# Performance work log

Measured on AMD Instinct MI355X. Metric: run time of the kernel, lower is better.

Reference implementation:

```python
import jax, jax.numpy as jnp
import numpy as np

E = 768      # embed_size
H = 12       # heads
L = 4        # num_length (stacked blocks)
N = 3072     # sequence length (and max_length)
FF = 4 * E   # feed-forward hidden
EPS = 1e-5


def layer_norm(x, g, b):
    mu = jnp.mean(x, axis=-1, keepdims=True)
    var = jnp.mean((x - mu) ** 2, axis=-1, keepdims=True)
    return (x - mu) / jnp.sqrt(var + EPS) * g + b


def setup_inputs() -> dict:
    key = jax.random.key(0)
    ks = jax.random.split(key, 12)
    inp = {
        "x": jax.random.normal(ks[0], (1, N, 768), dtype=jnp.float32),
        "mask": jnp.ones((1, N), dtype=jnp.int32),
        # 0.05 scale so word_encoding outputs have |.|>1 and survive the .long() truncation
        "W_word": jax.random.normal(ks[1], (E, 768), dtype=jnp.float32) * 0.05,
        "b_word": jnp.zeros((E,), dtype=jnp.float32),
        "pos_emb": jax.random.normal(ks[2], (N, E), dtype=jnp.float32),
        "Wq": jax.random.normal(ks[3], (L, E, E), dtype=jnp.float32) * 0.02,
        "Wk": jax.random.normal(ks[4], (L, E, E), dtype=jnp.float32) * 0.02,
        "Wv": jax.random.normal(ks[5], (L, E, E), dtype=jnp.float32) * 0.02,
        "Wo": jax.random.normal(ks[6], (L, E, E), dtype=jnp.float32) * 0.02,
        "W1": jax.random.normal(ks[7], (L, FF, E), dtype=jnp.float32) * 0.02,
        "b1": jnp.zeros((L, FF), dtype=jnp.float32),
        "W2": jax.random.normal(ks[8], (L, E, FF), dtype=jnp.float32) * 0.02,
        "b2": jnp.zeros((L, E), dtype=jnp.float32),
        "g1": jnp.ones((L, E), dtype=jnp.float32),
        "beta1": jnp.zeros((L, E), dtype=jnp.float32),
        "g2": jnp.ones((L, E), dtype=jnp.float32),
        "beta2": jnp.zeros((L, E), dtype=jnp.float32),
    }
    return inp


def reference(x, mask, W_word, b_word, pos_emb, Wq, Wk, Wv, Wo,
              W1, b1, W2, b2, g1, beta1, g2, beta2):
    # mask is squeezed then passed, but the original uses a non-inplace
    # masked_fill whose result is discarded -> mask has NO effect on the math.
    xs = x[0]                                # [N, 768]
    h = xs @ W_word.T + b_word               # word_encoding -> [N, E]
    h = jnp.trunc(h)                         # faithful to `x = x.long()` (cast truncation)
    n = h.shape[0]
    out = (h + pos_emb[:n])[None]            # [1, N, E]; dropout is identity (eval)
    d = E // H
    scale = jnp.asarray(E ** 0.5, out.dtype)  # softmax scaled by sqrt(embed_size)
    for l in range(L):
        q = (out @ Wq[l].T).reshape(1, n, H, d)
        k = (out @ Wk[l].T).reshape(1, n, H, d)
        v = (out @ Wv[l].T).reshape(1, n, H, d)
        energy = jnp.einsum('nqhd,nkhd->nhqk', q, k)      # [1, H, N, N]
        attn = jax.nn.softmax(energy / scale, axis=3)
        a = jnp.einsum('nhqk,nkhd->nqhd', attn, v).reshape(1, n, E) @ Wo[l].T
        xm = layer_norm(a + out, g1[l], beta1[l])
        y = jax.nn.relu(xm @ W1[l].T + b1[l]) @ W2[l].T + b2[l]
        out = layer_norm(xm + y, g2[l], beta2[l])
    return jnp.mean(out, axis=1, keepdims=True)          # [1, 1, E]
```

## Files before the change

kernel.cpp:

```cpp
#include <hip/hip_runtime.h>

#define E_  768
#define N_  3072
#define L_  4
#define H_  12
#define FF_ 3072
#define LDQKV 2304
#define SCL_ 0.052058744f

typedef short bf16x8 __attribute__((ext_vector_type(8)));
typedef short s16x4  __attribute__((ext_vector_type(4)));
typedef float f32x4  __attribute__((ext_vector_type(4)));
typedef _Float16 f16x4 __attribute__((ext_vector_type(4)));
typedef _Float16 f16x8 __attribute__((ext_vector_type(8)));

__device__ __forceinline__ short f2bf(float f) {
  union { float f; unsigned u; } v; v.f = f;
  unsigned r = v.u + 0x7fffu + ((v.u >> 16) & 1u);
  return (short)(r >> 16);
}
__device__ __forceinline__ float bf2f(short s) {
  union { unsigned u; float f; } v; v.u = ((unsigned)(unsigned short)s) << 16;
  return v.f;
}

__device__ __forceinline__ void gld_lds16(const void* g, void* l) {
  __builtin_amdgcn_global_load_lds(
      (const __attribute__((address_space(1))) unsigned int*)g,
      (__attribute__((address_space(3))) unsigned int*)l, 16, 0, 0);
}

__global__ __launch_bounds__(256) void gemm_bt_kernel(
    const short* __restrict__ A, const short* __restrict__ B,
    const float* __restrict__ bias, float* __restrict__ Cf,
    short* __restrict__ Cb, int M, int Nd, int K, int relu)
{
  (void)M;
  alignas(16) __shared__ short As[128 * 32];
  alignas(16) __shared__ short Bs[128 * 32];
  const int tid = threadIdx.x;
  const int w = tid >> 6, lane = tid & 63;
  const int quad = lane >> 4, cl = lane & 15;
  const int wr = w >> 1, wc = w & 1;
  const int row0 = blockIdx.y * 128, col0 = blockIdx.x * 128;
  const int srow = lane >> 2;
  const int scol = (((lane & 3) ^ ((lane >> 3) & 3)) * 8);
  const int rsw = (quad ^ ((cl >> 1) & 3)) * 8;
  const f32x4 fz = {0.f, 0.f, 0.f, 0.f};
  f32x4 acc[4][4];
#pragma unroll
  for (int i = 0; i < 4; i++)
#pragma unroll
    for (int j = 0; j < 4; j++) acc[i][j] = fz;

  const int nk = K >> 5;
  for (int kt = 0; kt < nk; kt++) {
    const int k0 = kt << 5;
#pragma unroll
    for (int i = 0; i < 2; i++) {
      const int chunk = w * 2 + i;
      gld_lds16(A + (size_t)(row0 + chunk * 16 + srow) * K + k0 + scol, As + chunk * 512);
      gld_lds16(B + (size_t)(col0 + chunk * 16 + srow) * K + k0 + scol, Bs + chunk * 512);
    }
    __syncthreads();
    bf16x8 af[4], bfr[4];
#pragma unroll
    for (int mt = 0; mt < 4; mt++)
      af[mt] = *(const bf16x8*)(As + (wr * 64 + mt * 16 + cl) * 32 + rsw);
#pragma unroll
    for (int nt = 0; nt < 4; nt++)
      bfr[nt] = *(const bf16x8*)(Bs + (wc * 64 + nt * 16 + cl) * 32 + rsw);
#pragma unroll
    for (int mt = 0; mt < 4; mt++)
#pragma unroll
      for (int nt = 0; nt < 4; nt++)
        acc[mt][nt] = __builtin_amdgcn_mfma_f32_16x16x32_bf16(af[mt], bfr[nt], acc[mt][nt], 0, 0, 0);
    __syncthreads();
  }
#pragma unroll
  for (int mt = 0; mt < 4; mt++)
#pragma unroll
    for (int nt = 0; nt < 4; nt++) {
      const int col = col0 + wc * 64 + nt * 16 + cl;
      const float bv = bias ? bias[col] : 0.f;
#pragma unroll
      for (int r = 0; r < 4; r++) {
        const int row = row0 + wr * 64 + mt * 16 + quad * 4 + r;
        float v2 = acc[mt][nt][r] + bv;
        if (relu) v2 = fmaxf(v2, 0.f);
        if (Cf) Cf[(size_t)row * Nd + col] = v2;
        if (Cb) Cb[(size_t)row * Nd + col] = f2bf(v2);
      }
    }
}

__global__ __launch_bounds__(256) void vtrans_kernel(const short* __restrict__ QKV,
                                                     _Float16* __restrict__ Vt)
{
  __shared__ _Float16 T[64 * 80];
  const int tid = threadIdx.x;
  const int n0 = blockIdx.x * 64, hoff = blockIdx.y * 64;
#pragma unroll
  for (int i = 0; i < 2; i++) {
    const int cidx = tid + i * 256;
    const int r = cidx >> 3, c0 = (cidx & 7) * 8;
    const bf16x8 v = *(const bf16x8*)(QKV + (size_t)(n0 + r) * LDQKV + 1536 + hoff + c0);
#pragma unroll
    for (int j = 0; j < 8; j++) T[r * 80 + c0 + j] = (_Float16)bf2f(v[j]);
  }
  __syncthreads();
#pragma unroll
  for (int i = 0; i < 2; i++) {
    const int cidx = tid + i * 256;
    const int d = cidx >> 3, c0 = (cidx & 7) * 8;
    f16x8 o;
#pragma unroll
    for (int j = 0; j < 8; j++) o[j] = T[(c0 + j) * 80 + d];
    *(f16x8*)(Vt + (size_t)(hoff + d) * N_ + n0 + c0) = o;
  }
}

__global__ __launch_bounds__(256) void flash_kernel(
    const short* __restrict__ QKV, const _Float16* __restrict__ Vt,
    float* __restrict__ Op, float* __restrict__ Ml)
{
  alignas(16) __shared__ short Ks[64 * 64];
  alignas(16) __shared__ _Float16 Vs[64 * 64];
  const int tid = threadIdx.x;
  const int w = tid >> 6, lane = tid & 63;
  const int quad = lane >> 4, cl = lane & 15;
  const int q0 = blockIdx.x * 64, h = blockIdx.y, s = blockIdx.z;
  const int hoff = h * 64;
  const f32x4 fz = {0.f, 0.f, 0.f, 0.f};
  const int qrow = q0 + w * 16 + cl;
  const short* qp = QKV + (size_t)qrow * LDQKV + hoff;
  const bf16x8 bq0 = *(const bf16x8*)(qp + quad * 8);
  const bf16x8 bq1 = *(const bf16x8*)(qp + 32 + quad * 8);

  const int strow = lane >> 3;
  const int stcol = ((lane & 7) ^ strow) * 8;
  const short* kp0 = QKV + (size_t)(s * 768 + w * 16 + strow) * LDQKV + 768 + hoff + stcol;
  const short* kp1 = kp0 + 8 * LDQKV;
  const _Float16* vp0 = Vt + (size_t)(hoff + w * 16 + strow) * N_ + s * 768 + stcol;
  const _Float16* vp1 = vp0 + 8 * N_;
  short* ksd = Ks + w * 1024;
  _Float16* vsd = Vs + w * 1024;

  const int swz = cl & 7;
  const short* kf0 = Ks + cl * 64 + ((quad ^ swz) * 8);
  const short* kf1 = Ks + cl * 64 + (((quad + 4) ^ swz) * 8);
  const _Float16* vf0 = Vs + cl * 64 + (((0 + (quad >> 1)) ^ swz) * 8) + (quad & 1) * 4;
  const _Float16* vf1 = Vs + cl * 64 + (((2 + (quad >> 1)) ^ swz) * 8) + (quad & 1) * 4;
  const _Float16* vf2 = Vs + cl * 64 + (((4 + (quad >> 1)) ^ swz) * 8) + (quad & 1) * 4;
  const _Float16* vf3 = Vs + cl * 64 + (((6 + (quad >> 1)) ^ swz) * 8) + (quad & 1) * 4;

  f32x4 Oa[4];
#pragma unroll
  for (int t = 0; t < 4; t++) Oa[t] = fz;
  float m = -1e30f, l = 0.f;

  for (int kb = 0; kb < 12; kb++) {
    gld_lds16(kp0, ksd);
    gld_lds16(kp1, ksd + 512);
    gld_lds16(vp0, vsd);
    gld_lds16(vp1, vsd + 512);
    kp0 += 64 * LDQKV; kp1 += 64 * LDQKV; vp0 += 64; vp1 += 64;
    __syncthreads();
    f32x4 S[4];
#pragma unroll
    for (int t = 0; t < 4; t++) {
      const bf16x8 ak0 = *(const bf16x8*)(kf0 + t * 1024);
      const bf16x8 ak1 = *(const bf16x8*)(kf1 + t * 1024);
      f32x4 z = fz;
      z = __builtin_amdgcn_mfma_f32_16x16x32_bf16(ak0, bq0, z, 0, 0, 0);
      S[t] = __builtin_amdgcn_mfma_f32_16x16x32_bf16(ak1, bq1, z, 0, 0, 0);
    }
    float mloc = -1e30f;
#pragma unroll
    for (int t = 0; t < 4; t++)
#pragma unroll
      for (int r = 0; r < 4; r++) mloc = fmaxf(mloc, S[t][r]);
    mloc = fmaxf(mloc, __shfl_xor(mloc, 16));
    mloc = fmaxf(mloc, __shfl_xor(mloc, 32));
    const float mn = fmaxf(m, mloc);
    const float alpha = exp2f(m - mn);
    m = mn;
    float rs = 0.f;
#pragma unroll
    for (int t = 0; t < 4; t++)
#pragma unroll
      for (int r = 0; r < 4; r++) {
        const float pp = exp2f(S[t][r] - m);
        S[t][r] = pp; rs += pp;
      }
    rs += __shfl_xor(rs, 16);
    rs += __shfl_xor(rs, 32);
    l = l * alpha + rs;
#pragma unroll
    for (int t = 0; t < 4; t++)
#pragma unroll
      for (int r = 0; r < 4; r++) Oa[t][r] *= alpha;
    f16x4 pf[4];
#pragma unroll
    for (int kt = 0; kt < 4; kt++)
#pragma unroll
      for (int j = 0; j < 4; j++) pf[kt][j] = (_Float16)S[kt][j];
#pragma unroll
    for (int td = 0; td < 4; td++) {
      Oa[td] = __builtin_amdgcn_mfma_f32_16x16x16f16(*(const f16x4*)(vf0 + td * 1024), pf[0], Oa[td], 0, 0, 0);
      Oa[td] = __builtin_amdgcn_mfma_f32_16x16x16f16(*(const f16x4*)(vf1 + td * 1024), pf[1], Oa[td], 0, 0, 0);
      Oa[td] = __builtin_amdgcn_mfma_f32_16x16x16f16(*(const f16x4*)(vf2 + td * 1024), pf[2], Oa[td], 0, 0, 0);
      Oa[td] = __builtin_amdgcn_mfma_f32_16x16x16f16(*(const f16x4*)(vf3 + td * 1024), pf[3], Oa[td], 0, 0, 0);
    }
    __syncthreads();
  }
  float* op = Op + ((size_t)s * N_ + qrow) * E_ + hoff;
#pragma unroll
  for (int td = 0; td < 4; td++)
#pragma unroll
    for (int r = 0; r < 4; r++)
      op[td * 16 + quad * 4 + r] = Oa[td][r];
  if (quad == 0) {
    const size_t idx = (((size_t)s * H_ + h) * N_ + qrow) * 2;
    Ml[idx] = m; Ml[idx + 1] = l;
  }
}

__global__ __launch_bounds__(256) void merge_kernel(
    const float* __restrict__ Op, const float* __restrict__ Ml,
    short* __restrict__ atb)
{
  const int idx = blockIdx.x * 256 + threadIdx.x;
  const int n = idx / 192, c4 = idx % 192;
  const int e0 = c4 * 4, h = e0 >> 6;
  float mm[4], ll[4];
#pragma unroll
  for (int s = 0; s < 4; s++) {
    const size_t mi = (((size_t)s * H_ + h) * N_ + n) * 2;
    mm[s] = Ml[mi]; ll[s] = Ml[mi + 1];
  }
  const float M = fmaxf(fmaxf(mm[0], mm[1]), fmaxf(mm[2], mm[3]));
  f32x4 num = {0.f, 0.f, 0.f, 0.f};
  float den = 0.f;
#pragma unroll
  for (int s = 0; s < 4; s++) {
    const float ws = exp2f(mm[s] - M);
    den += ws * ll[s];
    const f32x4 o = *(const f32x4*)(Op + ((size_t)s * N_ + n) * E_ + e0);
#pragma unroll
    for (int j = 0; j < 4; j++) num[j] += ws * o[j];
  }
  const float inv = 1.f / den;
  s16x4 ob;
#pragma unroll
  for (int j = 0; j < 4; j++) ob[j] = f2bf(num[j] * inv);
  *(s16x4*)(atb + (size_t)n * E_ + e0) = ob;
}

__global__ __launch_bounds__(256) void wordenc_kernel(
    const float* __restrict__ x, const float* __restrict__ Ww,
    const float* __restrict__ bw, const float* __restrict__ pos,
    float* __restrict__ of, short* __restrict__ ob)
{
  alignas(16) __shared__ float Xs[16 * 68];
  alignas(16) __shared__ float Wsh[16 * 68];
  const int tid = threadIdx.x;
  const int tx = tid & 15, ty = tid >> 4;
  const int row0 = blockIdx.y * 64, col0 = blockIdx.x * 64;
  const int lr = tid >> 2, lc = (tid & 3) * 4;
  float acc[4][4];
#pragma unroll
  for (int i = 0; i < 4; i++)
#pragma unroll
    for (int j = 0; j < 4; j++) acc[i][j] = 0.f;
  for (int k0 = 0; k0 < E_; k0 += 16) {
    const f32x4 xa = *(const f32x4*)(x + (size_t)(row0 + lr) * E_ + k0 + lc);
    const f32x4 wa = *(const f32x4*)(Ww + (size_t)(col0 + lr) * E_ + k0 + lc);
    __syncthreads();
#pragma unroll
    for (int q = 0; q < 4; q++) {
      Xs[(lc + q) * 68 + lr] = xa[q];
      Wsh[(lc + q) * 68 + lr] = wa[q];
    }
    __syncthreads();
#pragma unroll
    for (int kk = 0; kk < 16; kk++) {
      const f32x4 a4 = *(const f32x4*)(Xs + kk * 68 + ty * 4);
      const f32x4 b4 = *(const f32x4*)(Wsh + kk * 68 + tx * 4);
#pragma unroll
      for (int i = 0; i < 4; i++)
#pragma unroll
        for (int j = 0; j < 4; j++) acc[i][j] += a4[i] * b4[j];
    }
  }
#pragma unroll
  for (int i = 0; i < 4; i++) {
    const int rr = row0 + ty * 4 + i;
#pragma unroll
    for (int j = 0; j < 4; j++) {
      const int cc = col0 + tx * 4 + j;
      const float h = truncf(acc[i][j] + bw[cc]);
      const float o = h + pos[(size_t)rr * E_ + cc];
      of[(size_t)rr * E_ + cc] = o;
      ob[(size_t)rr * E_ + cc] = f2bf(o);
    }
  }
}

__global__ __launch_bounds__(256) void resid_ln_kernel(
    const float* __restrict__ a, const float* __restrict__ b,
    const float* __restrict__ g, const float* __restrict__ bet,
    float* __restrict__ of, short* __restrict__ ob)
{
  const int row = blockIdx.x, tid = threadIdx.x;
  const int w = tid >> 6, lane = tid & 63;
  __shared__ float red[8];
  const size_t base = (size_t)row * E_;
  float v[3]; float s = 0.f;
#pragma unroll
  for (int j = 0; j < 3; j++) {
    const int cc = tid + j * 256;
    v[j] = a[base + cc] + b[base + cc];
    s += v[j];
  }
#pragma unroll
  for (int msk = 1; msk < 64; msk <<= 1) s += __shfl_xor(s, msk);
  if (lane == 0) red[w] = s;
  __syncthreads();
  const float mean = (red[0] + red[1] + red[2] + red[3]) * (1.f / E_);
  float s2 = 0.f;
#pragma unroll
  for (int j = 0; j < 3; j++) { const float d = v[j] - mean; s2 += d * d; }
#pragma unroll
  for (int msk = 1; msk < 64; msk <<= 1) s2 += __shfl_xor(s2, msk);
  if (lane == 0) red[4 + w] = s2;
  __syncthreads();
  const float var = (red[4] + red[5] + red[6] + red[7]) * (1.f / E_);
  const float rstd = rsqrtf(var + 1e-5f);
#pragma unroll
  for (int j = 0; j < 3; j++) {
    const int cc = tid + j * 256;
    const float o = (v[j] - mean) * rstd * g[cc] + bet[cc];
    of[base + cc] = o;
    ob[base + cc] = f2bf(o);
  }
}

__global__ void f2b_kernel(const float* __restrict__ s, short* __restrict__ d, int n4)
{
  const int i = blockIdx.x * 256 + threadIdx.x;
  if (i < n4) {
    const f32x4 v = *(const f32x4*)(s + (size_t)i * 4);
    s16x4 o;
#pragma unroll
    for (int q = 0; q < 4; q++) o[q] = f2bf(v[q]);
    *(s16x4*)(d + (size_t)i * 4) = o;
  }
}

__global__ void f2b3_kernel(const float* __restrict__ s, short* __restrict__ d,
                            int which, float scale)
{
  const int i = blockIdx.x * 256 + threadIdx.x;
  if (i < 589824) {
    const size_t e4 = (size_t)i * 4;
    const int lidx = (int)(e4 / (E_ * E_));
    const size_t rem = e4 % (E_ * E_);
    const f32x4 v = *(const f32x4*)(s + e4);
    s16x4 o;
#pragma unroll
    for (int q = 0; q < 4; q++) o[q] = f2bf(v[q] * scale);
    *(s16x4*)(d + ((size_t)lidx * 3 + which) * E_ * E_ + rem) = o;
  }
}

__global__ void colmean_kernel(const float* __restrict__ src, float* __restrict__ out)
{
  const int c = blockIdx.x * 256 + threadIdx.x;
  const int r0 = blockIdx.y * 128;
  float s = 0.f;
  for (int r = 0; r < 128; r++) s += src[(size_t)(r0 + r) * E_ + c];
  atomicAdd(&out[c], s * (1.f / N_));
}

extern "C" void kernel_launch(void* const* d_in, const int* in_sizes, int n_in,
                              void* d_out, int out_size, void* d_ws, size_t ws_size,
                              hipStream_t stream)
{
  (void)in_sizes; (void)n_in; (void)out_size; (void)ws_size;
  const float* x     = (const float*)d_in[0];
  const float* Wword = (const float*)d_in[2];
  const float* bword = (const float*)d_in[3];
  const float* pos   = (const float*)d_in[4];
  const float* Wq    = (const float*)d_in[5];
  const float* Wk    = (const float*)d_in[6];
  const float* Wv    = (const float*)d_in[7];
  const float* Wo    = (const float*)d_in[8];
  const float* W1    = (const float*)d_in[9];
  const float* b1    = (const float*)d_in[10];
  const float* W2    = (const float*)d_in[11];
  const float* b2    = (const float*)d_in[12];
  const float* g1    = (const float*)d_in[13];
  const float* be1   = (const float*)d_in[14];
  const float* g2    = (const float*)d_in[15];
  const float* be2   = (const float*)d_in[16];

  char* p = (char*)d_ws;
  auto take = [&](size_t bytes) { char* q = p; p += (bytes + 255) & ~(size_t)255; return q; };
  const size_t EE = (size_t)E_ * E_;
  const size_t NE = (size_t)N_ * E_;
  const size_t FE = (size_t)FF_ * E_;

  short* wqkv_b = (short*)take(L_ * 3 * EE * 2);
  short* wo_b   = (short*)take(L_ * EE * 2);
  short* w1_b   = (short*)take(L_ * FE * 2);
  short* w2_b   = (short*)take(L_ * FE * 2);
  float* outf   = (float*)take(NE * 4);
  short* outb   = (short*)take(NE * 2);
  float* xmf    = (float*)take(NE * 4);
  short* xmb    = (short*)take(NE * 2);
  short* qkvb   = (short*)take((size_t)N_ * LDQKV * 2);
  char*  big    = take(4 * NE * 4);
  float* Ml     = (float*)take((size_t)4 * H_ * N_ * 2 * 4);

  float* Op   = (float*)big;
  short* y1b  = (short*)big;
  float* tmpf = (float*)(big + (size_t)N_ * FF_ * 2);
  _Float16* vtb = (_Float16*)xmf;
  short* atb  = outb;

  auto cvt = [&](const float* src, short* dst, size_t n) {
    const int n4 = (int)(n / 4);
    f2b_kernel<<<dim3((n4 + 255) / 256), dim3(256), 0, stream>>>(src, dst, n4);
  };
  f2b3_kernel<<<dim3(2304), dim3(256), 0, stream>>>(Wq, wqkv_b, 0, SCL_);
  f2b3_kernel<<<dim3(2304), dim3(256), 0, stream>>>(Wk, wqkv_b, 1, 1.f);
  f2b3_kernel<<<dim3(2304), dim3(256), 0, stream>>>(Wv, wqkv_b, 2, 1.f);
  cvt(Wo, wo_b, L_ * EE);
  cvt(W1, w1_b, L_ * FE);
  cvt(W2, w2_b, L_ * FE);

  wordenc_kernel<<<dim3(12, 48), dim3(256), 0, stream>>>(x, Wword, bword, pos, outf, outb);

  for (int l = 0; l < L_; l++) {
    gemm_bt_kernel<<<dim3(18, 24), dim3(256), 0, stream>>>(outb, wqkv_b + l * 3 * EE, nullptr, nullptr, qkvb, N_, LDQKV, E_, 0);
    vtrans_kernel<<<dim3(48, 12), dim3(256), 0, stream>>>(qkvb, vtb);
    flash_kernel<<<dim3(48, 12, 4), dim3(256), 0, stream>>>(qkvb, vtb, Op, Ml);
    merge_kernel<<<dim3(2304), dim3(256), 0, stream>>>(Op, Ml, atb);
    gemm_bt_kernel<<<dim3(6, 24), dim3(256), 0, stream>>>(atb, wo_b + l * EE, nullptr, tmpf, nullptr, N_, E_, E_, 0);
    resid_ln_kernel<<<dim3(N_), dim3(256), 0, stream>>>(tmpf, outf, g1 + l * E_, be1 + l * E_, xmf, xmb);
    gemm_bt_kernel<<<dim3(24, 24), dim3(256), 0, stream>>>(xmb, w1_b + l * FE, b1 + l * FF_, nullptr, y1b, N_, FF_, E_, 1);
    gemm_bt_kernel<<<dim3(6, 24), dim3(256), 0, stream>>>(y1b, w2_b + l * FE, b2 + l * E_, tmpf, nullptr, N_, E_, FF_, 0);
    resid_ln_kernel<<<dim3(N_), dim3(256), 0, stream>>>(xmf, tmpf, g2 + l * E_, be2 + l * E_, outf, outb);
  }
  hipMemsetAsync(d_out, 0, E_ * sizeof(float), stream);
  colmean_kernel<<<dim3(3, 24), dim3(256), 0, stream>>>(outf, (float*)d_out);
}
```

Before: 1.238 ms.

## Split-K narrow GEMMs, merge weight conversions, and run word encoding on MFMA

The Wo and W2 GEMMs, whose 6x24 grids give few blocks, are split along K into two z-slices that write separate fp32 partials. The following residual-layernorm kernel sums the partials and applies the bias, which raises occupancy on those launches. The fp32 SIMT word-encoding GEMM is replaced by a bf16 MFMA GEMM that uses hi/lo splitting (hi*hi + lo*hi + hi*lo) to keep enough precision for the truncation. All weight conversions are fused into one prep kernel launch. The risks are extra partial-buffer traffic and possible precision mismatches after trunc where the split-bf16 product differs from fp32.

```diff
diff --git a/kernel.cpp b/kernel.cpp
--- a/kernel.cpp
+++ b/kernel.cpp
@@ -33,9 +33,9 @@
 __global__ __launch_bounds__(256) void gemm_bt_kernel(
     const short* __restrict__ A, const short* __restrict__ B,
     const float* __restrict__ bias, float* __restrict__ Cf,
-    short* __restrict__ Cb, int M, int Nd, int K, int relu)
-{
-  (void)M;
+    short* __restrict__ Cb, int Nd, int lda, int ldb,
+    int kcnt, size_t czstride, int relu)
+{
   alignas(16) __shared__ short As[128 * 32];
   alignas(16) __shared__ short Bs[128 * 32];
   const int tid = threadIdx.x;
@@ -43,6 +43,9 @@
   const int quad = lane >> 4, cl = lane & 15;
   const int wr = w >> 1, wc = w & 1;
   const int row0 = blockIdx.y * 128, col0 = blockIdx.x * 128;
+  const int koff = blockIdx.z * kcnt;
+  A += koff; B += koff;
+  if (Cf) Cf += (size_t)blockIdx.z * czstride;
   const int srow = lane >> 2;
   const int scol = (((lane & 3) ^ ((lane >> 3) & 3)) * 8);
   const int rsw = (quad ^ ((cl >> 1) & 3)) * 8;
@@ -53,14 +56,14 @@
 #pragma unroll
     for (int j = 0; j < 4; j++) acc[i][j] = fz;
 
-  const int nk = K >> 5;
+  const int nk = kcnt >> 5;
   for (int kt = 0; kt < nk; kt++) {
     const int k0 = kt << 5;
 #pragma unroll
     for (int i = 0; i < 2; i++) {
       const int chunk = w * 2 + i;
-      gld_lds16(A + (size_t)(row0 + chunk * 16 + srow) * K + k0 + scol, As + chunk * 512);
-      gld_lds16(B + (size_t)(col0 + chunk * 16 + srow) * K + k0 + scol, Bs + chunk * 512);
+      gld_lds16(A + (size_t)(row0 + chunk * 16 + srow) * lda + k0 + scol, As + chunk * 512);
+      gld_lds16(B + (size_t)(col0 + chunk * 16 + srow) * ldb + k0 + scol, Bs + chunk * 512);
     }
     __syncthreads();
     bf16x8 af[4], bfr[4];
@@ -257,59 +260,33 @@
   *(s16x4*)(atb + (size_t)n * E_ + e0) = ob;
 }
 
-__global__ __launch_bounds__(256) void wordenc_kernel(
-    const float* __restrict__ x, const float* __restrict__ Ww,
+__global__ __launch_bounds__(256) void wordenc_fin_kernel(
+    const float* __restrict__ p0, const float* __restrict__ p1,
     const float* __restrict__ bw, const float* __restrict__ pos,
     float* __restrict__ of, short* __restrict__ ob)
 {
-  alignas(16) __shared__ float Xs[16 * 68];
-  alignas(16) __shared__ float Wsh[16 * 68];
-  const int tid = threadIdx.x;
-  const int tx = tid & 15, ty = tid >> 4;
-  const int row0 = blockIdx.y * 64, col0 = blockIdx.x * 64;
-  const int lr = tid >> 2, lc = (tid & 3) * 4;
-  float acc[4][4];
-#pragma unroll
-  for (int i = 0; i < 4; i++)
-#pragma unroll
-    for (int j = 0; j < 4; j++) acc[i][j] = 0.f;
-  for (int k0 = 0; k0 < E_; k0 += 16) {
-    const f32x4 xa = *(const f32x4*)(x + (size_t)(row0 + lr) * E_ + k0 + lc);
-    const f32x4 wa = *(const f32x4*)(Ww + (size_t)(col0 + lr) * E_ + k0 + lc);
-    __syncthreads();
-#pragma unroll
-    for (int q = 0; q < 4; q++) {
-      Xs[(lc + q) * 68 + lr] = xa[q];
-      Wsh[(lc + q) * 68 + lr] = wa[q];
-    }
-    __syncthreads();
-#pragma unroll
-    for (int kk = 0; kk < 16; kk++) {
-      const f32x4 a4 = *(const f32x4*)(Xs + kk * 68 + ty * 4);
-      const f32x4 b4 = *(const f32x4*)(Wsh + kk * 68 + tx * 4);
-#pragma unroll
-      for (int i = 0; i < 4; i++)
-#pragma unroll
-        for (int j = 0; j < 4; j++) acc[i][j] += a4[i] * b4[j];
-    }
-  }
-#pragma unroll
-  for (int i = 0; i < 4; i++) {
-    const int rr = row0 + ty * 4 + i;
-#pragma unroll
-    for (int j = 0; j < 4; j++) {
-      const int cc = col0 + tx * 4 + j;
-      const float h = truncf(acc[i][j] + bw[cc]);
-      const float o = h + pos[(size_t)rr * E_ + cc];
-      of[(size_t)rr * E_ + cc] = o;
-      ob[(size_t)rr * E_ + cc] = f2bf(o);
-    }
-  }
+  const int idx = blockIdx.x * 256 + threadIdx.x;
+  const size_t e4 = (size_t)idx * 4;
+  const int cc = (int)(e4 % E_);
+  const f32x4 a = *(const f32x4*)(p0 + e4);
+  const f32x4 b = *(const f32x4*)(p1 + e4);
+  const f32x4 bwv = *(const f32x4*)(bw + cc);
+  const f32x4 pv = *(const f32x4*)(pos + e4);
+  f32x4 o; s16x4 obv;
+#pragma unroll
+  for (int j = 0; j < 4; j++) {
+    o[j] = truncf(a[j] + b[j] + bwv[j]) + pv[j];
+    obv[j] = f2bf(o[j]);
+  }
+  *(f32x4*)(of + e4) = o;
+  *(s16x4*)(ob + e4) = obv;
 }
 
 __global__ __launch_bounds__(256) void resid_ln_kernel(
-    const float* __restrict__ a, const float* __restrict__ b,
+    const float* __restrict__ a0, const float* __restrict__ a1,
+    const float* __restrict__ b,
     const float* __restrict__ g, const float* __restrict__ bet,
+    const float* __restrict__ bias,
     float* __restrict__ of, short* __restrict__ ob)
 {
   const int row = blockIdx.x, tid = threadIdx.x;
@@ -320,8 +297,10 @@
 #pragma unroll
   for (int j = 0; j < 3; j++) {
     const int cc = tid + j * 256;
-    v[j] = a[base + cc] + b[base + cc];
-    s += v[j];
+    float t = a0[base + cc] + a1[base + cc] + b[base + cc];
+    if (bias) t += bias[cc];
+    v[j] = t;
+    s += t;
   }
 #pragma unroll
   for (int msk = 1; msk < 64; msk <<= 1) s += __shfl_xor(s, msk);
@@ -346,31 +325,97 @@
   }
 }
 
-__global__ void f2b_kernel(const float* __restrict__ s, short* __restrict__ d, int n4)
-{
-  const int i = blockIdx.x * 256 + threadIdx.x;
-  if (i < n4) {
-    const f32x4 v = *(const f32x4*)(s + (size_t)i * 4);
-    s16x4 o;
-#pragma unroll
-    for (int q = 0; q < 4; q++) o[q] = f2bf(v[q]);
-    *(s16x4*)(d + (size_t)i * 4) = o;
-  }
-}
-
-__global__ void f2b3_kernel(const float* __restrict__ s, short* __restrict__ d,
-                            int which, float scale)
-{
-  const int i = blockIdx.x * 256 + threadIdx.x;
-  if (i < 589824) {
-    const size_t e4 = (size_t)i * 4;
+__global__ __launch_bounds__(256) void prep_kernel(
+    const float* __restrict__ Wq, const float* __restrict__ Wk,
+    const float* __restrict__ Wv, const float* __restrict__ Wo,
+    const float* __restrict__ W1, const float* __restrict__ W2,
+    const float* __restrict__ Ww, const float* __restrict__ x,
+    short* __restrict__ wqkv, short* __restrict__ wo_b,
+    short* __restrict__ w1_b, short* __restrict__ w2_b,
+    short* __restrict__ whl, short* __restrict__ xhl)
+{
+  int g = blockIdx.x * 256 + threadIdx.x;
+  const int EEg = 589824;
+  const int FEg = 2359296;
+  if (g < 3 * EEg) {
+    const int which = g / EEg;
+    const int gi = g - which * EEg;
+    const float* src = which == 0 ? Wq : (which == 1 ? Wk : Wv);
+    const float scale = which == 0 ? SCL_ : 1.f;
+    const size_t e4 = (size_t)gi * 4;
     const int lidx = (int)(e4 / (E_ * E_));
     const size_t rem = e4 % (E_ * E_);
-    const f32x4 v = *(const f32x4*)(s + e4);
+    const f32x4 v = *(const f32x4*)(src + e4);
     s16x4 o;
 #pragma unroll
     for (int q = 0; q < 4; q++) o[q] = f2bf(v[q] * scale);
-    *(s16x4*)(d + ((size_t)lidx * 3 + which) * E_ * E_ + rem) = o;
+    *(s16x4*)(wqkv + ((size_t)lidx * 3 + which) * E_ * E_ + rem) = o;
+    return;
+  }
+  g -= 3 * EEg;
+  if (g < EEg) {
+    const size_t e4 = (size_t)g * 4;
+    const f32x4 v = *(const f32x4*)(Wo + e4);
+    s16x4 o;
+#pragma unroll
+    for (int q = 0; q < 4; q++) o[q] = f2bf(v[q]);
+    *(s16x4*)(wo_b + e4) = o;
+    return;
+  }
+  g -= EEg;
+  if (g < FEg) {
+    const size_t e4 = (size_t)g * 4;
+    const f32x4 v = *(const f32x4*)(W1 + e4);
+    s16x4 o;
+#pragma unroll
+    for (int q = 0; q < 4; q++) o[q] = f2bf(v[q]);
+    *(s16x4*)(w1_b + e4) = o;
+    return;
+  }
+  g -= FEg;
+  if (g < FEg) {
+    const size_t e4 = (size_t)g * 4;
+    const f32x4 v = *(const f32x4*)(W2 + e4);
+    s16x4 o;
+#pragma unroll
+    for (int q = 0; q < 4; q++) o[q] = f2bf(v[q]);
+    *(s16x4*)(w2_b + e4) = o;
+    return;
+  }
+  g -= FEg;
+  if (g < 147456) {
+    const size_t e4 = (size_t)g * 4;
+    const int c = (int)(e4 / E_);
+    const int k = (int)(e4 % E_);
+    const f32x4 v = *(const f32x4*)(Ww + e4);
+    s16x4 hi, lo;
+#pragma unroll
+    for (int q = 0; q < 4; q++) {
+      hi[q] = f2bf(v[q]);
+      lo[q] = f2bf(v[q] - bf2f(hi[q]));
+    }
+    short* base = whl + (size_t)c * LDQKV + k;
+    *(s16x4*)(base) = hi;
+    *(s16x4*)(base + 768) = hi;
+    *(s16x4*)(base + 1536) = lo;
+    return;
+  }
+  g -= 147456;
+  {
+    const size_t e4 = (size_t)g * 4;
+    const int n = (int)(e4 / E_);
+    const int k = (int)(e4 % E_);
+    const f32x4 v = *(const f32x4*)(x + e4);
+    s16x4 hi, lo;
+#pragma unroll
+    for (int q = 0; q < 4; q++) {
+      hi[q] = f2bf(v[q]);
+      lo[q] = f2bf(v[q] - bf2f(hi[q]));
+    }
+    short* base = xhl + (size_t)n * LDQKV + k;
+    *(s16x4*)(base) = hi;
+    *(s16x4*)(base + 768) = lo;
+    *(s16x4*)(base + 1536) = hi;
   }
 }
 
@@ -415,43 +460,47 @@
   short* wo_b   = (short*)take(L_ * EE * 2);
   short* w1_b   = (short*)take(L_ * FE * 2);
   short* w2_b   = (short*)take(L_ * FE * 2);
+  short* whl    = (short*)take((size_t)E_ * LDQKV * 2);
   float* outf   = (float*)take(NE * 4);
   short* outb   = (short*)take(NE * 2);
   float* xmf    = (float*)take(NE * 4);
   short* xmb    = (short*)take(NE * 2);
   short* qkvb   = (short*)take((size_t)N_ * LDQKV * 2);
-  char*  big    = take(4 * NE * 4);
+  float* Op     = (float*)take(4 * NE * 4);
   float* Ml     = (float*)take((size_t)4 * H_ * N_ * 2 * 4);
 
-  float* Op   = (float*)big;
-  short* y1b  = (short*)big;
-  float* tmpf = (float*)(big + (size_t)N_ * FF_ * 2);
+  short* xhl  = qkvb;
+  short* y1b  = (short*)Op;
+  float* part0 = Op + 2 * NE;
+  float* part1 = Op + 3 * NE;
   _Float16* vtb = (_Float16*)xmf;
   short* atb  = outb;
 
-  auto cvt = [&](const float* src, short* dst, size_t n) {
-    const int n4 = (int)(n / 4);
-    f2b_kernel<<<dim3((n4 + 255) / 256), dim3(256), 0, stream>>>(src, dst, n4);
-  };
-  f2b3_kernel<<<dim3(2304), dim3(256), 0, stream>>>(Wq, wqkv_b, 0, SCL_);
-  f2b3_kernel<<<dim3(2304), dim3(256), 0, stream>>>(Wk, wqkv_b, 1, 1.f);
-  f2b3_kernel<<<dim3(2304), dim3(256), 0, stream>>>(Wv, wqkv_b, 2, 1.f);
-  cvt(Wo, wo_b, L_ * EE);
-  cvt(W1, w1_b, L_ * FE);
-  cvt(W2, w2_b, L_ * FE);
-
-  wordenc_kernel<<<dim3(12, 48), dim3(256), 0, stream>>>(x, Wword, bword, pos, outf, outb);
+  prep_kernel<<<dim3(30528), dim3(256), 0, stream>>>(
+      Wq, Wk, Wv, Wo, W1, W2, Wword, x,
+      wqkv_b, wo_b, w1_b, w2_b, whl, xhl);
+
+  gemm_bt_kernel<<<dim3(6, 24, 2), dim3(256), 0, stream>>>(
+      xhl, whl, nullptr, Op, nullptr, E_, LDQKV, LDQKV, 1152, NE, 0);
+  wordenc_fin_kernel<<<dim3(2304), dim3(256), 0, stream>>>(
+      Op, Op + NE, bword, pos, outf, outb);
 
   for (int l = 0; l < L_; l++) {
-    gemm_bt_kernel<<<dim3(18, 24), dim3(256), 0, stream>>>(outb, wqkv_b + l * 3 * EE, nullptr, nullptr, qkvb, N_, LDQKV, E_, 0);
+    gemm_bt_kernel<<<dim3(18, 24, 1), dim3(256), 0, stream>>>(
+        outb, wqkv_b + l * 3 * EE, nullptr, nullptr, qkvb, LDQKV, E_, E_, E_, 0, 0);
     vtrans_kernel<<<dim3(48, 12), dim3(256), 0, stream>>>(qkvb, vtb);
     flash_kernel<<<dim3(48, 12, 4), dim3(256), 0, stream>>>(qkvb, vtb, Op, Ml);
     merge_kernel<<<dim3(2304), dim3(256), 0, stream>>>(Op, Ml, atb);
-    gemm_bt_kernel<<<dim3(6, 24), dim3(256), 0, stream>>>(atb, wo_b + l * EE, nullptr, tmpf, nullptr, N_, E_, E_, 0);
-    resid_ln_kernel<<<dim3(N_), dim3(256), 0, stream>>>(tmpf, outf, g1 + l * E_, be1 + l * E_, xmf, xmb);
-    gemm_bt_kernel<<<dim3(24, 24), dim3(256), 0, stream>>>(xmb, w1_b + l * FE, b1 + l * FF_, nullptr, y1b, N_, FF_, E_, 1);
-    gemm_bt_kernel<<<dim3(6, 24), dim3(256), 0, stream>>>(y1b, w2_b + l * FE, b2 + l * E_, tmpf, nullptr, N_, E_, FF_, 0);
-    resid_ln_kernel<<<dim3(N_), dim3(256), 0, stream>>>(xmf, tmpf, g2 + l * E_, be2 + l * E_, outf, outb);
+    gemm_bt_kernel<<<dim3(6, 24, 2), dim3(256), 0, stream>>>(
+        atb, wo_b + l * EE, nullptr, part0, nullptr, E_, E_, E_, 384, NE, 0);
+    resid_ln_kernel<<<dim3(N_), dim3(256), 0, stream>>>(
+        part0, part1, outf, g1 + l * E_, be1 + l * E_, nullptr, xmf, xmb);
+    gemm_bt_kernel<<<dim3(24, 24, 1), dim3(256), 0, stream>>>(
+        xmb, w1_b + l * FE, b1 + l * FF_, nullptr, y1b, FF_, E_, E_, E_, 0, 1);
+    gemm_bt_kernel<<<dim3(6, 24, 2), dim3(256), 0, stream>>>(
+        y1b, w2_b + l * FE, nullptr, part0, nullptr, E_, FF_, FF_, 1536, NE, 0);
+    resid_ln_kernel<<<dim3(N_), dim3(256), 0, stream>>>(
+        part0, part1, xmf, g2 + l * E_, be2 + l * E_, b2 + l * E_, outf, outb);
   }
   hipMemsetAsync(d_out, 0, E_ * sizeof(float), stream);
   colmean_kernel<<<dim3(3, 24), dim3(256), 0, stream>>>(outf, (float*)d_out);
```

After: 1.116 ms. -9.9%, faster.
